# Kernel optimization log

Hardware: AMD Instinct MI355X
Metric: run time of the kernel (lower is better)

## Reference

```python
import jax, jax.numpy as jnp
import numpy as np

B, T, F, H = 4096, 512, 32, 32  # batch, seq_len, input_size, hidden_size


def setup_inputs() -> dict:
    key = jax.random.key(0)
    ks = jax.random.split(key, 7)
    s = 1.0 / np.sqrt(H)  # torch LSTM/Linear init scale
    return {
        "x": jax.random.normal(ks[0], (B, T, F), dtype=jnp.float32),
        "W_ih": jax.random.uniform(ks[1], (4 * H, F), minval=-s, maxval=s, dtype=jnp.float32),
        "W_hh": jax.random.uniform(ks[2], (4 * H, H), minval=-s, maxval=s, dtype=jnp.float32),
        "b_ih": jax.random.uniform(ks[3], (4 * H,), minval=-s, maxval=s, dtype=jnp.float32),
        "b_hh": jax.random.uniform(ks[4], (4 * H,), minval=-s, maxval=s, dtype=jnp.float32),
        "W_fc": jax.random.uniform(ks[5], (1, H), minval=-s, maxval=s, dtype=jnp.float32),
        "b_fc": jax.random.uniform(ks[6], (1,), minval=-s, maxval=s, dtype=jnp.float32),
    }


def _lstm_last_hidden(x, W_ih, W_hh, b_ih, b_hh):
    # Precompute input-to-gate projections for all timesteps in one GEMM.
    # Gate packing order (PyTorch): i, f, g, o.
    h_dim = W_hh.shape[1]
    xg = jnp.einsum("btf,gf->btg", x, W_ih) + (b_ih + b_hh)  # [B,T,4H]
    xg = jnp.transpose(xg, (1, 0, 2))  # [T,B,4H] for scan over time

    def step(carry, g_x):
        h, c = carry
        gates = g_x + h @ W_hh.T  # [B,4H]
        i = jax.nn.sigmoid(gates[:, 0 * h_dim:1 * h_dim])
        f = jax.nn.sigmoid(gates[:, 1 * h_dim:2 * h_dim])
        g = jnp.tanh(gates[:, 2 * h_dim:3 * h_dim])
        o = jax.nn.sigmoid(gates[:, 3 * h_dim:4 * h_dim])
        c_new = f * c + i * g
        h_new = o * jnp.tanh(c_new)
        return (h_new, c_new), None

    h0 = jnp.zeros((x.shape[0], h_dim), dtype=x.dtype)
    c0 = jnp.zeros_like(h0)
    (h_last, _), _ = jax.lax.scan(step, (h0, c0), xg)
    return h_last  # [B,H]


def reference(x, W_ih, W_hh, b_ih, b_hh, W_fc, b_fc):
    h_last = _lstm_last_hidden(x, W_ih, W_hh, b_ih, b_hh)
    # Dropout is identity in eval mode (reference baseline is deterministic).
    logits = h_last @ W_fc.T + b_fc  # [B,1]
    return jnp.squeeze(logits, -1)  # [B]
```

## Files before the change

kernel.cpp:

```cpp
#include <hip/hip_runtime.h>
#include <stdint.h>


typedef _Float16 half8 __attribute__((ext_vector_type(8)));
typedef __attribute__((ext_vector_type(4))) float float4v;

#define T_LEN 512
#define B_ALL 4096
#define ROWS 16
#define NBLK (B_ALL / ROWS)
#define P 40

__global__ __launch_bounds__(512, 2) void lstm_fused_kernel(
    const float* __restrict__ x,
    const float* __restrict__ W_ih,
    const float* __restrict__ W_hh,
    const float* __restrict__ b_ih,
    const float* __restrict__ b_hh,
    const float* __restrict__ W_fc,
    const float* __restrict__ b_fc,
    float* __restrict__ out)
{
    const int tid  = threadIdx.x;
    const int wv   = tid >> 6;
    const int lane = tid & 63;
    const int col  = lane & 15;
    const int q    = lane >> 4;
    const int k0   = q * 8;
    const int b0   = blockIdx.x * ROWS;
    const int e    = 4 * wv + q;

    __shared__ __align__(16) _Float16 hs[2][ROWS][P];
    __shared__ __align__(16) _Float16 xs[2][ROWS][P];

    half8 wih, whh;
    {
        const int gt   = col & 3;
        const int gmem = gt * 32 + (4 * wv + (col >> 2));
        const float gs = (gt == 2) ? 2.88539008f : -1.44269504f;
        const float* wr = W_ih + gmem * 32 + k0;
        const float* hr = W_hh + gmem * 32 + k0;
        #pragma unroll
        for (int i = 0; i < 8; ++i) {
            wih[i] = (_Float16)(wr[i] * gs);
            whh[i] = (_Float16)(hr[i] * gs);
        }
    }
    float4v bias4;
    #pragma unroll
    for (int r = 0; r < 4; ++r) {
        const float gsr = (r == 2) ? 2.88539008f : -1.44269504f;
        bias4[r] = (b_ih[r * 32 + e] + b_hh[r * 32 + e]) * gsr;
    }

    float c = 0.f;

    const int sr = tid >> 5;
    const int sk = tid & 31;
    const float* xsrc = x + ((size_t)(b0 + sr) * T_LEN) * 32 + sk;

    float xA, xB;
    {
        xs[0][sr][sk] = (_Float16)xsrc[0];
        xA = xsrc[32];
        xB = xsrc[64];
        hs[0][sr][sk] = (_Float16)0.f;
    }
    __syncthreads();

    const float4v zero4 = {0.f, 0.f, 0.f, 0.f};

    #define STEP(PPAR, XREG, TT)                                                \
    {                                                                           \
        const half8 ax = *(const half8*)&xs[PPAR][col][k0];                     \
        const half8 ah = *(const half8*)&hs[PPAR][col][k0];                     \
                                               \
        float4v a1 = bias4, a2 = zero4;                                         \
        a1 = __builtin_amdgcn_mfma_f32_16x16x32_f16(wih, ax, a1, 0, 0, 0);      \
        a2 = __builtin_amdgcn_mfma_f32_16x16x32_f16(whh, ah, a2, 0, 0, 0);      \
        {                \
            xs[PPAR ^ 1][sr][sk] = (_Float16)XREG;                              \
            int tn = (TT) + 3; if (tn >= T_LEN) tn = T_LEN - 1;                 \
            XREG = xsrc[(size_t)tn * 32];                                       \
        }                                                                       \
        const float4v g = a1 + a2;                                              \
         \
          \
        const float Ai = __builtin_amdgcn_exp2f(g[0]);                          \
        const float Af = __builtin_amdgcn_exp2f(g[1]);                          \
        const float Bg = __builtin_amdgcn_exp2f(g[2]);                          \
        const float Ao = __builtin_amdgcn_exp2f(g[3]);                          \
        const float pI = 1.0f + Ai;                                             \
        const float pG = 1.0f + Bg;                                             \
        const float pF = 1.0f + Af;                                             \
        const float pIG = pI * pG;                                              \
        const float num = c * pIG + (Bg - 1.0f) * pF;                           \
        c = num * __builtin_amdgcn_rcpf(pF * pIG);                              \
        const float cc = fminf(fmaxf(c, -16.0f), 16.0f);                        \
        const float C2 = __builtin_amdgcn_exp2f(cc * 2.88539008f);              \
        const float r3 = __builtin_amdgcn_rcpf((1.0f + Ao) * (1.0f + C2));      \
        const float hv = (C2 - 1.0f) * r3;                                      \
        hs[PPAR ^ 1][col][e] = (_Float16)hv;                                    \
        __syncthreads();                                                        \
    }

    for (int t = 0; t < T_LEN; t += 2) {
        STEP(0, xA, t)
        STEP(1, xB, t + 1)
    }
    #undef STEP

    if (tid < ROWS) {
        float s = b_fc[0];
        #pragma unroll
        for (int cc2 = 0; cc2 < 32; ++cc2) {
            s += (float)hs[0][tid][cc2] * W_fc[cc2];
        }
        out[b0 + tid] = s;
    }
}

extern "C" void kernel_launch(void* const* d_in, const int* in_sizes, int n_in,
                              void* d_out, int out_size, void* d_ws, size_t ws_size,
                              hipStream_t stream) {
    const float* x    = (const float*)d_in[0];
    const float* W_ih = (const float*)d_in[1];
    const float* W_hh = (const float*)d_in[2];
    const float* b_ih = (const float*)d_in[3];
    const float* b_hh = (const float*)d_in[4];
    const float* W_fc = (const float*)d_in[5];
    const float* b_fc = (const float*)d_in[6];
    float* out = (float*)d_out;

    lstm_fused_kernel<<<dim3(NBLK), dim3(512), 0, stream>>>(
        x, W_ih, W_hh, b_ih, b_hh, W_fc, b_fc, out);
}
```

Baseline: 141.4 us.

## Software-pipeline input projection MFMA one step ahead and chain into recurrent MFMA

Computes the next timestep's input-projection MFMA during the current step and feeds it as the accumulator of the recurrent W_hh MFMA. This takes the x-side MFMA and the vector add off the serial critical path. The x staging buffer grows to four slots and prefetch distance increases to keep the indexing consistent. The cost is more shared memory and slightly more live registers.

Result: faster. 137.2 us (-3.0%).

```diff
diff --git a/kernel.cpp b/kernel.cpp
--- a/kernel.cpp
+++ b/kernel.cpp
@@ -31,7 +31,7 @@
     const int e    = 4 * wv + q;
 
     __shared__ __align__(16) _Float16 hs[2][ROWS][P];
-    __shared__ __align__(16) _Float16 xs[2][ROWS][P];
+    __shared__ __align__(16) _Float16 xs[4][ROWS][P];
 
     half8 wih, whh;
     {
@@ -62,34 +62,42 @@
     float xA, xB;
     {
         xs[0][sr][sk] = (_Float16)xsrc[0];
-        xA = xsrc[32];
-        xB = xsrc[64];
+        xs[1][sr][sk] = (_Float16)xsrc[32];
+        xs[2][sr][sk] = (_Float16)xsrc[64];
         hs[0][sr][sk] = (_Float16)0.f;
+        xA = xsrc[3 * 32];
+        xB = xsrc[4 * 32];
     }
     __syncthreads();
 
-    const float4v zero4 = {0.f, 0.f, 0.f, 0.f};
+    float4v a1c;
+    {
+        const half8 ax0 = *(const half8*)&xs[0][col][k0];
+        a1c = __builtin_amdgcn_mfma_f32_16x16x32_f16(wih, ax0, bias4, 0, 0, 0);
+    }
 
     #define STEP(PPAR, XREG, TT)                                                \
     {                                                                           \
-        const half8 ax = *(const half8*)&xs[PPAR][col][k0];                     \
-        const half8 ah = *(const half8*)&hs[PPAR][col][k0];                     \
-                                               \
-        float4v a1 = bias4, a2 = zero4;                                         \
-        a1 = __builtin_amdgcn_mfma_f32_16x16x32_f16(wih, ax, a1, 0, 0, 0);      \
-        a2 = __builtin_amdgcn_mfma_f32_16x16x32_f16(whh, ah, a2, 0, 0, 0);      \
-        {                \
-            xs[PPAR ^ 1][sr][sk] = (_Float16)XREG;                              \
-            int tn = (TT) + 3; if (tn >= T_LEN) tn = T_LEN - 1;                 \
+        const int xq = ((TT) + 1) & 3;                                          \
+        const int xw = ((TT) + 3) & 3;                                          \
+        const half8 ah  = *(const half8*)&hs[PPAR][col][k0];      \
+        const half8 axn = *(const half8*)&xs[xq][col][k0];     \
+                           \
+        const float4v acc =                                                     \
+            __builtin_amdgcn_mfma_f32_16x16x32_f16(whh, ah, a1c, 0, 0, 0);      \
+                                \
+        a1c = __builtin_amdgcn_mfma_f32_16x16x32_f16(wih, axn, bias4, 0, 0, 0); \
+        {                   \
+            xs[xw][sr][sk] = (_Float16)XREG;                                    \
+            int tn = (TT) + 5; if (tn >= T_LEN) tn = T_LEN - 1;                 \
             XREG = xsrc[(size_t)tn * 32];                                       \
         }                                                                       \
-        const float4v g = a1 + a2;                                              \
          \
           \
-        const float Ai = __builtin_amdgcn_exp2f(g[0]);                          \
-        const float Af = __builtin_amdgcn_exp2f(g[1]);                          \
-        const float Bg = __builtin_amdgcn_exp2f(g[2]);                          \
-        const float Ao = __builtin_amdgcn_exp2f(g[3]);                          \
+        const float Ai = __builtin_amdgcn_exp2f(acc[0]);                        \
+        const float Af = __builtin_amdgcn_exp2f(acc[1]);                        \
+        const float Bg = __builtin_amdgcn_exp2f(acc[2]);                        \
+        const float Ao = __builtin_amdgcn_exp2f(acc[3]);                        \
         const float pI = 1.0f + Ai;                                             \
         const float pG = 1.0f + Bg;                                             \
         const float pF = 1.0f + Af;                                             \
```
